# Kernel tuning notes

Hardware: AMD Instinct MI355X
Metric: run time of the kernel (lower is better)

The kernel has to match this reference:

```python
import jax, jax.numpy as jnp
import numpy as np

B, N, M, DIM, H, DH = 2, 2048, 2048, 512, 8, 64
INNER = H * DH  # 512


def setup_inputs() -> dict:
    key = jax.random.key(0)
    ks = jax.random.split(key, 9)
    s = 0.02
    return {
        "x": jax.random.normal(ks[0], (B, N, DIM), jnp.float32),
        "x1": jax.random.normal(ks[1], (B, M, DIM), jnp.float32),
        "attn_mat": jax.random.normal(ks[2], (B, H, N, M), jnp.float32),
        "dots_para": jax.random.uniform(ks[3], (1,), jnp.float32),
        "mat_para": jax.random.uniform(ks[4], (1,), jnp.float32),
        "W_qv": jax.random.normal(ks[5], (DIM, 2 * INNER), jnp.float32) * s,
        "W_k": jax.random.normal(ks[6], (DIM, INNER), jnp.float32) * s,
        "W_out": jax.random.normal(ks[7], (INNER, DIM), jnp.float32) * s,
        "b_out": jax.random.normal(ks[8], (DIM,), jnp.float32) * s,
    }


def _split_heads(t):
    # [b, n, h*d] -> [b, h, n, d]
    b, n, _ = t.shape
    return t.reshape(b, n, H, DH).transpose(0, 2, 1, 3)


def reference(x, x1, attn_mat, dots_para, mat_para, W_qv, W_k, W_out, b_out):
    scale = DH ** -0.5
    qv = x @ W_qv                      # [b, n, 2*inner]
    q, v = jnp.split(qv, 2, axis=-1)
    q = _split_heads(q)                # [b, h, n, d]
    v = _split_heads(v)                # [b, h, n, d]
    k = _split_heads(x1 @ W_k)         # [b, h, m, d]
    dots = jnp.einsum("bhnd,bhmd->bhnm", q, k) * scale
    dots = dots * dots_para + attn_mat * mat_para
    attn = jax.nn.softmax(dots, axis=-1)
    out = jnp.einsum("bhnm,bhmd->bhnd", attn, v)
    out = out.transpose(0, 2, 1, 3).reshape(x.shape[0], x.shape[1], INNER)
    return out @ W_out + b_out
```

## Files before the change

kernel.cpp:

```cpp
#include <hip/hip_runtime.h>
#include <hip/hip_bf16.h>

#define NB 2048
#define MB 2048

typedef __attribute__((ext_vector_type(8))) short short8;
typedef __attribute__((ext_vector_type(4))) float floatx4;

__device__ __forceinline__ unsigned short f2bf(float f) {
    union { float f; unsigned int u; } v; v.f = f;
    unsigned int r = (v.u + 0x7FFFu + ((v.u >> 16) & 1u)) >> 16;
    return (unsigned short)r;
}

__device__ __forceinline__ int swz(int row, int k) {
    return (row << 6) + ((((k >> 3) ^ (row & 7))) << 3) + (k & 7);
}
__device__ __forceinline__ int vswz(int row, int k) {
    return (row << 6) + ((((k >> 3) ^ (row & 7) ^ ((row >> 3) & 7))) << 3) + (k & 7);
}

__launch_bounds__(256)
__global__ void cvt_bf16(const float* __restrict__ in, unsigned short* __restrict__ out, int n4) {
    int idx = blockIdx.x * 256 + threadIdx.x;
    if (idx >= n4) return;
    float4 d = *(const float4*)(in + (size_t)idx * 4);
    uint2 o;
    o.x = (unsigned int)f2bf(d.x) | ((unsigned int)f2bf(d.y) << 16);
    o.y = (unsigned int)f2bf(d.z) | ((unsigned int)f2bf(d.w) << 16);
    *(uint2*)(out + (size_t)idx * 4) = o;
}

__launch_bounds__(256)
__global__ void transpose_cvt(const float* __restrict__ W, unsigned short* __restrict__ Wt,
                              int K, int N) {
    __shared__ float t[64][65];
    const int tid = threadIdx.x;
    const int k0 = blockIdx.x * 64, n0 = blockIdx.y * 64;
#pragma unroll
    for (int p = 0; p < 4; p++) {
        int idx = p * 256 + tid;
        int kr = idx >> 4, c4 = (idx & 15) << 2;
        float4 d = *(const float4*)(W + (size_t)(k0 + kr) * N + n0 + c4);
        t[kr][c4 + 0] = d.x; t[kr][c4 + 1] = d.y; t[kr][c4 + 2] = d.z; t[kr][c4 + 3] = d.w;
    }
    __syncthreads();
#pragma unroll
    for (int p = 0; p < 4; p++) {
        int idx = p * 256 + tid;
        int nr = idx >> 4, k4 = (idx & 15) << 2;
        uint2 o;
        o.x = (unsigned int)f2bf(t[k4 + 0][nr]) | ((unsigned int)f2bf(t[k4 + 1][nr]) << 16);
        o.y = (unsigned int)f2bf(t[k4 + 2][nr]) | ((unsigned int)f2bf(t[k4 + 3][nr]) << 16);
        *(uint2*)(Wt + (size_t)(n0 + nr) * K + k0 + k4) = o;
    }
}

template <int OUT_BF16>
__launch_bounds__(256)
__global__ void gemm_bt(const unsigned short* __restrict__ A, const unsigned short* __restrict__ Bt,
                        const float* __restrict__ bias, void* __restrict__ Cp, int Nc) {
    __shared__ short Al[64 * 64];
    __shared__ short Bl[64 * 64];

    const int tid = threadIdx.x;
    const int w = tid >> 6, lane = tid & 63;
    const int quad = lane >> 4, c16 = lane & 15;
    const int wr = (w >> 1) * 32, wc = (w & 1) * 32;
    const int m0 = blockIdx.x * 64, n0 = blockIdx.y * 64;

    floatx4 acc[2][2];
#pragma unroll
    for (int i = 0; i < 2; i++)
#pragma unroll
        for (int j = 0; j < 2; j++) acc[i][j] = floatx4{0.f, 0.f, 0.f, 0.f};

    for (int kk = 0; kk < 512; kk += 64) {
        __syncthreads();
#pragma unroll
        for (int p = 0; p < 2; p++) {
            int id = p * 256 + tid;
            int row = id >> 3, c8 = (id & 7) << 3;
            *(uint4*)&Al[swz(row, c8)] = *(const uint4*)(A + (size_t)(m0 + row) * 512 + kk + c8);
            *(uint4*)&Bl[swz(row, c8)] = *(const uint4*)(Bt + (size_t)(n0 + row) * 512 + kk + c8);
        }
        __syncthreads();
#pragma unroll
        for (int kc = 0; kc < 2; kc++) {
            short8 af[2], bf[2];
#pragma unroll
            for (int mt = 0; mt < 2; mt++)
                af[mt] = *(const short8*)&Al[swz(wr + mt * 16 + c16, kc * 32 + quad * 8)];
#pragma unroll
            for (int nt = 0; nt < 2; nt++)
                bf[nt] = *(const short8*)&Bl[swz(wc + nt * 16 + c16, kc * 32 + quad * 8)];
#pragma unroll
            for (int mt = 0; mt < 2; mt++)
#pragma unroll
                for (int nt = 0; nt < 2; nt++)
                    acc[mt][nt] = __builtin_amdgcn_mfma_f32_16x16x32_bf16(af[mt], bf[nt], acc[mt][nt], 0, 0, 0);
        }
    }
#pragma unroll
    for (int mt = 0; mt < 2; mt++)
#pragma unroll
        for (int nt = 0; nt < 2; nt++)
#pragma unroll
            for (int r = 0; r < 4; r++) {
                int row = m0 + wr + mt * 16 + quad * 4 + r;
                int col = n0 + wc + nt * 16 + c16;
                float v = acc[mt][nt][r];
                if (OUT_BF16) {
                    ((unsigned short*)Cp)[(size_t)row * Nc + col] = f2bf(v);
                } else {
                    ((float*)Cp)[(size_t)row * Nc + col] = v + bias[col];
                }
            }
}

__launch_bounds__(256)
__global__ void flash_attn(const unsigned short* __restrict__ qv,
                           const unsigned short* __restrict__ kb,
                           const float* __restrict__ attn_mat,
                           const float* __restrict__ dots_para,
                           const float* __restrict__ mat_para,
                           float* __restrict__ Opart,
                           float* __restrict__ lpart) {
    __shared__ short Qs[64 * 64];
    __shared__ short Ks[64 * 64];
    __shared__ short Vs[64 * 64];
    __shared__ short Ps[4][16 * 64];

    const int tid = threadIdx.x, w = tid >> 6, lane = tid & 63;
    const int quad = lane >> 4, c16 = lane & 15;
    const int q0 = blockIdx.x * 64;
    const int bh = blockIdx.y;
    const int sp = blockIdx.z;
    const int b = bh >> 3, h = bh & 7;
    const int ms = sp * (MB / 2);

    const float mp = mat_para[0];
    const float sdp = dots_para[0] * 0.125f;

    for (int id = tid; id < 512; id += 256) {
        int r = id >> 3, c = id & 7;
        *(uint4*)&Qs[swz(r, c * 8)] =
            *(const uint4*)(qv + (size_t)(b * NB + q0 + r) * 1024 + h * 64 + c * 8);
    }
    __syncthreads();
    short8 qf0 = *(const short8*)&Qs[swz(w * 16 + c16, quad * 8)];
    short8 qf1 = *(const short8*)&Qs[swz(w * 16 + c16, 32 + quad * 8)];

    floatx4 O[4];
    float l[4] = {0.f, 0.f, 0.f, 0.f};
#pragma unroll
    for (int dt = 0; dt < 4; dt++) O[dt] = floatx4{0.f, 0.f, 0.f, 0.f};

    const float* am_base = attn_mat + ((size_t)bh * NB + q0 + w * 16 + quad * 4) * MB;

    for (int m0 = ms; m0 < ms + MB / 2; m0 += 64) {
        __syncthreads();
        for (int id = tid; id < 512; id += 256) {
            int r = id >> 3, c = id & 7;
            *(uint4*)&Ks[swz(r, c * 8)] =
                *(const uint4*)(kb + (size_t)(b * MB + m0 + r) * 512 + h * 64 + c * 8);
        }
        for (int id = tid; id < 512; id += 256) {
            int r = id >> 3, c = id & 7;
            uint4 d = *(const uint4*)(qv + (size_t)(b * NB + m0 + r) * 1024 + 512 + h * 64 + c * 8);
            Vs[vswz(c * 8 + 0, r)] = (short)(d.x & 0xffff);
            Vs[vswz(c * 8 + 1, r)] = (short)(d.x >> 16);
            Vs[vswz(c * 8 + 2, r)] = (short)(d.y & 0xffff);
            Vs[vswz(c * 8 + 3, r)] = (short)(d.y >> 16);
            Vs[vswz(c * 8 + 4, r)] = (short)(d.z & 0xffff);
            Vs[vswz(c * 8 + 5, r)] = (short)(d.z >> 16);
            Vs[vswz(c * 8 + 6, r)] = (short)(d.w & 0xffff);
            Vs[vswz(c * 8 + 7, r)] = (short)(d.w >> 16);
        }
        __syncthreads();

        float am[4][4];
#pragma unroll
        for (int t = 0; t < 4; t++)
#pragma unroll
            for (int r = 0; r < 4; r++)
                am[t][r] = am_base[(size_t)r * MB + m0 + t * 16 + c16];

        floatx4 S[4];
#pragma unroll
        for (int t = 0; t < 4; t++) {
            short8 kf0 = *(const short8*)&Ks[swz(t * 16 + c16, quad * 8)];
            short8 kf1 = *(const short8*)&Ks[swz(t * 16 + c16, 32 + quad * 8)];
            floatx4 s = floatx4{0.f, 0.f, 0.f, 0.f};
            s = __builtin_amdgcn_mfma_f32_16x16x32_bf16(qf0, kf0, s, 0, 0, 0);
            s = __builtin_amdgcn_mfma_f32_16x16x32_bf16(qf1, kf1, s, 0, 0, 0);
            S[t] = s;
        }

#pragma unroll
        for (int t = 0; t < 4; t++)
#pragma unroll
            for (int r = 0; r < 4; r++) {
                float p = __expf(fmaf(S[t][r], sdp, am[t][r] * mp));
                l[r] += p;
                Ps[w][swz(quad * 4 + r, t * 16 + c16)] = (short)f2bf(p);
            }
        __threadfence_block();
        short8 pf0 = *(const short8*)&Ps[w][swz(c16, quad * 8)];
        short8 pf1 = *(const short8*)&Ps[w][swz(c16, 32 + quad * 8)];

#pragma unroll
        for (int dt = 0; dt < 4; dt++) {
            short8 vf0 = *(const short8*)&Vs[vswz(dt * 16 + c16, quad * 8)];
            short8 vf1 = *(const short8*)&Vs[vswz(dt * 16 + c16, 32 + quad * 8)];
            O[dt] = __builtin_amdgcn_mfma_f32_16x16x32_bf16(pf0, vf0, O[dt], 0, 0, 0);
            O[dt] = __builtin_amdgcn_mfma_f32_16x16x32_bf16(pf1, vf1, O[dt], 0, 0, 0);
        }
    }

#pragma unroll
    for (int r = 0; r < 4; r++) {
        float s = l[r];
        s += __shfl_xor(s, 1);
        s += __shfl_xor(s, 2);
        s += __shfl_xor(s, 4);
        s += __shfl_xor(s, 8);
        l[r] = s;
    }
    if (c16 == 0) {
#pragma unroll
        for (int r = 0; r < 4; r++)
            lpart[((size_t)(sp * 16 + bh)) * NB + q0 + w * 16 + quad * 4 + r] = l[r];
    }
#pragma unroll
    for (int dt = 0; dt < 4; dt++)
#pragma unroll
        for (int r = 0; r < 4; r++) {
            size_t row = (size_t)sp * 4096 + b * NB + q0 + w * 16 + quad * 4 + r;
            Opart[row * 512 + h * 64 + dt * 16 + c16] = O[dt][r];
        }
}

__launch_bounds__(256)
__global__ void combine_splits(const float* __restrict__ Opart, const float* __restrict__ lpart,
                               unsigned short* __restrict__ ao) {
    int idx = blockIdx.x * 256 + threadIdx.x;
    int row = idx >> 7;
    int col = (idx & 127) << 2;
    int b = row >> 11, n = row & 2047, h = col >> 6;
    float l0 = lpart[(size_t)(b * 8 + h) * NB + n];
    float l1 = lpart[(size_t)(16 + b * 8 + h) * NB + n];
    float rinv = 1.0f / (l0 + l1);
    float4 o0 = *(const float4*)(Opart + (size_t)row * 512 + col);
    float4 o1 = *(const float4*)(Opart + ((size_t)4096 + row) * 512 + col);
    uint2 o;
    o.x = (unsigned int)f2bf((o0.x + o1.x) * rinv) | ((unsigned int)f2bf((o0.y + o1.y) * rinv) << 16);
    o.y = (unsigned int)f2bf((o0.z + o1.z) * rinv) | ((unsigned int)f2bf((o0.w + o1.w) * rinv) << 16);
    *(uint2*)(ao + (size_t)row * 512 + col) = o;
}

extern "C" void kernel_launch(void* const* d_in, const int* in_sizes, int n_in,
                              void* d_out, int out_size, void* d_ws, size_t ws_size,
                              hipStream_t stream) {
    const float* x         = (const float*)d_in[0];
    const float* x1        = (const float*)d_in[1];
    const float* attn_mat  = (const float*)d_in[2];
    const float* dots_para = (const float*)d_in[3];
    const float* mat_para  = (const float*)d_in[4];
    const float* W_qv      = (const float*)d_in[5];
    const float* W_k       = (const float*)d_in[6];
    const float* W_out     = (const float*)d_in[7];
    const float* b_out     = (const float*)d_in[8];
    float* out = (float*)d_out;

    unsigned short* xb    = (unsigned short*)d_ws;
    unsigned short* x1b   = xb    + (size_t)4096 * 512;
    unsigned short* qvbf  = x1b   + (size_t)4096 * 512;
    unsigned short* kbf   = qvbf  + (size_t)4096 * 1024;
    unsigned short* aobf  = kbf   + (size_t)4096 * 512;
    unsigned short* Wqvt  = aobf  + (size_t)4096 * 512;
    unsigned short* Wkt   = Wqvt  + (size_t)1024 * 512;
    unsigned short* Woutt = Wkt   + (size_t)512 * 512;
    float*          Opart = (float*)(Woutt + (size_t)512 * 512);
    float*          lpart = Opart + (size_t)2 * 4096 * 512;

    dim3 blk(256);
    cvt_bf16<<<2048, blk, 0, stream>>>(x, xb, 524288);
    cvt_bf16<<<2048, blk, 0, stream>>>(x1, x1b, 524288);
    transpose_cvt<<<dim3(8, 16), blk, 0, stream>>>(W_qv, Wqvt, 512, 1024);
    transpose_cvt<<<dim3(8, 8), blk, 0, stream>>>(W_k, Wkt, 512, 512);
    transpose_cvt<<<dim3(8, 8), blk, 0, stream>>>(W_out, Woutt, 512, 512);
    gemm_bt<1><<<dim3(64, 16), blk, 0, stream>>>(xb, Wqvt, nullptr, qvbf, 1024);
    gemm_bt<1><<<dim3(64, 8), blk, 0, stream>>>(x1b, Wkt, nullptr, kbf, 512);
    flash_attn<<<dim3(32, 16, 2), blk, 0, stream>>>(qvbf, kbf, attn_mat, dots_para, mat_para, Opart, lpart);
    combine_splits<<<2048, blk, 0, stream>>>(Opart, lpart, aobf);
    gemm_bt<0><<<dim3(64, 8), blk, 0, stream>>>(aobf, Woutt, b_out, out, 512);
}
```

Baseline: 464.6 us.

## Restructure attention with 128-row tiles, double-buffered K/V, 4 splits, fused prep/GEMM launches

Each flash-attention block now covers 128 query rows, two 16-row tiles per wave, so every K/V tile loaded into shared memory is reused twice. K/V and attn_mat loads are register-prefetched and shared memory is double-buffered, so the next tile's global loads overlap the current tile's MFMA work. exp is rewritten as exp2 with log2e folded into the scales. The key dimension is split four ways instead of two. The conversion, transpose and QV/K GEMM launches are merged into fewer kernels to cut launch overhead, at the cost of more partial-output traffic in the combine step and higher register pressure.

```diff
diff --git a/kernel.cpp b/kernel.cpp
--- a/kernel.cpp
+++ b/kernel.cpp
@@ -3,6 +3,8 @@
 
 #define NB 2048
 #define MB 2048
+#define SPLITS 4
+#define MSP (MB / SPLITS)
 
 typedef __attribute__((ext_vector_type(8))) short short8;
 typedef __attribute__((ext_vector_type(4))) float floatx4;
@@ -21,22 +23,34 @@
 }
 
 __launch_bounds__(256)
-__global__ void cvt_bf16(const float* __restrict__ in, unsigned short* __restrict__ out, int n4) {
-    int idx = blockIdx.x * 256 + threadIdx.x;
-    if (idx >= n4) return;
-    float4 d = *(const float4*)(in + (size_t)idx * 4);
-    uint2 o;
-    o.x = (unsigned int)f2bf(d.x) | ((unsigned int)f2bf(d.y) << 16);
-    o.y = (unsigned int)f2bf(d.z) | ((unsigned int)f2bf(d.w) << 16);
-    *(uint2*)(out + (size_t)idx * 4) = o;
-}
-
-__launch_bounds__(256)
-__global__ void transpose_cvt(const float* __restrict__ W, unsigned short* __restrict__ Wt,
-                              int K, int N) {
+__global__ void prep(const float* __restrict__ x, const float* __restrict__ x1,
+                     const float* __restrict__ Wqv, const float* __restrict__ Wk,
+                     const float* __restrict__ Wout,
+                     unsigned short* __restrict__ xb, unsigned short* __restrict__ x1b,
+                     unsigned short* __restrict__ Wqvt, unsigned short* __restrict__ Wkt,
+                     unsigned short* __restrict__ Woutt) {
     __shared__ float t[64][65];
-    const int tid = threadIdx.x;
-    const int k0 = blockIdx.x * 64, n0 = blockIdx.y * 64;
+    const int bid = blockIdx.x, tid = threadIdx.x;
+    if (bid < 2048) {
+        const float* in = bid < 1024 ? x : x1;
+        unsigned short* out = bid < 1024 ? xb : x1b;
+        size_t off = ((size_t)(bid & 1023) * 256 + tid) * 8;
+        float4 d0 = *(const float4*)(in + off);
+        float4 d1 = *(const float4*)(in + off + 4);
+        uint4 o;
+        o.x = (unsigned int)f2bf(d0.x) | ((unsigned int)f2bf(d0.y) << 16);
+        o.y = (unsigned int)f2bf(d0.z) | ((unsigned int)f2bf(d0.w) << 16);
+        o.z = (unsigned int)f2bf(d1.x) | ((unsigned int)f2bf(d1.y) << 16);
+        o.w = (unsigned int)f2bf(d1.z) | ((unsigned int)f2bf(d1.w) << 16);
+        *(uint4*)(out + off) = o;
+        return;
+    }
+    int tb = bid - 2048;
+    const float* W; unsigned short* Wt; int N;
+    if (tb < 128)      { W = Wqv;  Wt = Wqvt;  N = 1024; }
+    else if (tb < 192) { tb -= 128; W = Wk;   Wt = Wkt;   N = 512; }
+    else               { tb -= 192; W = Wout; Wt = Woutt; N = 512; }
+    const int k0 = (tb & 7) * 64, n0 = (tb >> 3) * 64;
 #pragma unroll
     for (int p = 0; p < 4; p++) {
         int idx = p * 256 + tid;
@@ -52,22 +66,20 @@
         uint2 o;
         o.x = (unsigned int)f2bf(t[k4 + 0][nr]) | ((unsigned int)f2bf(t[k4 + 1][nr]) << 16);
         o.y = (unsigned int)f2bf(t[k4 + 2][nr]) | ((unsigned int)f2bf(t[k4 + 3][nr]) << 16);
-        *(uint2*)(Wt + (size_t)(n0 + nr) * K + k0 + k4) = o;
+        *(uint2*)(Wt + (size_t)(n0 + nr) * 512 + k0 + k4) = o;
     }
 }
 
 template <int OUT_BF16>
-__launch_bounds__(256)
-__global__ void gemm_bt(const unsigned short* __restrict__ A, const unsigned short* __restrict__ Bt,
-                        const float* __restrict__ bias, void* __restrict__ Cp, int Nc) {
-    __shared__ short Al[64 * 64];
-    __shared__ short Bl[64 * 64];
-
+__device__ __forceinline__ void gemm64_body(const unsigned short* __restrict__ A,
+                                            const unsigned short* __restrict__ Bt,
+                                            const float* __restrict__ bias,
+                                            void* __restrict__ Cp, int Nc, int m0, int n0,
+                                            short* Al, short* Bl) {
     const int tid = threadIdx.x;
     const int w = tid >> 6, lane = tid & 63;
     const int quad = lane >> 4, c16 = lane & 15;
     const int wr = (w >> 1) * 32, wc = (w & 1) * 32;
-    const int m0 = blockIdx.x * 64, n0 = blockIdx.y * 64;
 
     floatx4 acc[2][2];
 #pragma unroll
@@ -119,6 +131,29 @@
 }
 
 __launch_bounds__(256)
+__global__ void gemm_qvk(const unsigned short* __restrict__ xb, const unsigned short* __restrict__ x1b,
+                         const unsigned short* __restrict__ Wqvt, const unsigned short* __restrict__ Wkt,
+                         unsigned short* __restrict__ qvbf, unsigned short* __restrict__ kbf) {
+    __shared__ short Al[64 * 64];
+    __shared__ short Bl[64 * 64];
+    int bid = blockIdx.x;
+    if (bid < 1024) {
+        gemm64_body<1>(xb, Wqvt, nullptr, qvbf, 1024, (bid & 63) * 64, (bid >> 6) * 64, Al, Bl);
+    } else {
+        bid -= 1024;
+        gemm64_body<1>(x1b, Wkt, nullptr, kbf, 512, (bid & 63) * 64, (bid >> 6) * 64, Al, Bl);
+    }
+}
+
+__launch_bounds__(256)
+__global__ void gemm_out(const unsigned short* __restrict__ A, const unsigned short* __restrict__ Bt,
+                         const float* __restrict__ bias, float* __restrict__ C) {
+    __shared__ short Al[64 * 64];
+    __shared__ short Bl[64 * 64];
+    gemm64_body<0>(A, Bt, bias, C, 512, blockIdx.x * 64, blockIdx.y * 64, Al, Bl);
+}
+
+__launch_bounds__(256)
 __global__ void flash_attn(const unsigned short* __restrict__ qv,
                            const unsigned short* __restrict__ kb,
                            const float* __restrict__ attn_mat,
@@ -126,119 +161,167 @@
                            const float* __restrict__ mat_para,
                            float* __restrict__ Opart,
                            float* __restrict__ lpart) {
-    __shared__ short Qs[64 * 64];
-    __shared__ short Ks[64 * 64];
-    __shared__ short Vs[64 * 64];
-    __shared__ short Ps[4][16 * 64];
+    __shared__ short QP[4][32 * 64];
+    __shared__ short Ks[2][64 * 64];
+    __shared__ short Vs[2][64 * 64];
 
     const int tid = threadIdx.x, w = tid >> 6, lane = tid & 63;
     const int quad = lane >> 4, c16 = lane & 15;
-    const int q0 = blockIdx.x * 64;
+    const int q0 = blockIdx.x * 128;
     const int bh = blockIdx.y;
     const int sp = blockIdx.z;
     const int b = bh >> 3, h = bh & 7;
-    const int ms = sp * (MB / 2);
-
-    const float mp = mat_para[0];
-    const float sdp = dots_para[0] * 0.125f;
-
-    for (int id = tid; id < 512; id += 256) {
+    const int ms = sp * MSP;
+
+    const float log2e = 1.4426950408889634f;
+    const float mp = mat_para[0] * log2e;
+    const float sdp = dots_para[0] * 0.125f * log2e;
+
+    short* QPf = (short*)QP;
+#pragma unroll
+    for (int p = 0; p < 4; p++) {
+        int id = p * 256 + tid;
         int r = id >> 3, c = id & 7;
-        *(uint4*)&Qs[swz(r, c * 8)] =
+        *(uint4*)&QPf[swz(r, c * 8)] =
             *(const uint4*)(qv + (size_t)(b * NB + q0 + r) * 1024 + h * 64 + c * 8);
     }
     __syncthreads();
-    short8 qf0 = *(const short8*)&Qs[swz(w * 16 + c16, quad * 8)];
-    short8 qf1 = *(const short8*)&Qs[swz(w * 16 + c16, 32 + quad * 8)];
-
-    floatx4 O[4];
-    float l[4] = {0.f, 0.f, 0.f, 0.f};
-#pragma unroll
-    for (int dt = 0; dt < 4; dt++) O[dt] = floatx4{0.f, 0.f, 0.f, 0.f};
-
-    const float* am_base = attn_mat + ((size_t)bh * NB + q0 + w * 16 + quad * 4) * MB;
-
-    for (int m0 = ms; m0 < ms + MB / 2; m0 += 64) {
+    short8 qf[2][2];
+#pragma unroll
+    for (int at = 0; at < 2; at++)
+#pragma unroll
+        for (int kc = 0; kc < 2; kc++)
+            qf[at][kc] = *(const short8*)&QPf[swz(w * 32 + at * 16 + c16, kc * 32 + quad * 8)];
+    short* Pw = &QPf[w * 2048];
+
+    const int sr = tid >> 3, sc = tid & 7;
+    uint4 kreg[2], vreg[2];
+    auto loadKV = [&](int m) {
+#pragma unroll
+        for (int p = 0; p < 2; p++) {
+            int r = p * 32 + sr;
+            kreg[p] = *(const uint4*)(kb + (size_t)(b * MB + m + r) * 512 + h * 64 + sc * 8);
+            vreg[p] = *(const uint4*)(qv + (size_t)(b * NB + m + r) * 1024 + 512 + h * 64 + sc * 8);
+        }
+    };
+    auto storeKV = [&](int bufi) {
+#pragma unroll
+        for (int p = 0; p < 2; p++) {
+            int r = p * 32 + sr;
+            *(uint4*)&Ks[bufi][swz(r, sc * 8)] = kreg[p];
+            uint4 d = vreg[p];
+            Vs[bufi][vswz(sc * 8 + 0, r)] = (short)(d.x & 0xffff);
+            Vs[bufi][vswz(sc * 8 + 1, r)] = (short)(d.x >> 16);
+            Vs[bufi][vswz(sc * 8 + 2, r)] = (short)(d.y & 0xffff);
+            Vs[bufi][vswz(sc * 8 + 3, r)] = (short)(d.y >> 16);
+            Vs[bufi][vswz(sc * 8 + 4, r)] = (short)(d.z & 0xffff);
+            Vs[bufi][vswz(sc * 8 + 5, r)] = (short)(d.z >> 16);
+            Vs[bufi][vswz(sc * 8 + 6, r)] = (short)(d.w & 0xffff);
+            Vs[bufi][vswz(sc * 8 + 7, r)] = (short)(d.w >> 16);
+        }
+    };
+    const float* amp = attn_mat + ((size_t)bh * NB + q0 + w * 32 + quad * 4) * MB + c16;
+    float amr[2][4][4];
+    auto loadAM = [&](int m0_) {
+#pragma unroll
+        for (int at = 0; at < 2; at++)
+#pragma unroll
+            for (int r = 0; r < 4; r++)
+#pragma unroll
+                for (int t = 0; t < 4; t++)
+                    amr[at][t][r] = amp[(size_t)(at * 16 + r) * MB + m0_ + t * 16];
+    };
+
+    loadKV(ms);
+    storeKV(0);
+    loadKV(ms + 64 < ms + MSP ? ms + 64 : ms);
+    loadAM(ms);
+
+    floatx4 O[2][4];
+    float l[2][4];
+#pragma unroll
+    for (int at = 0; at < 2; at++)
+#pragma unroll
+        for (int i = 0; i < 4; i++) { O[at][i] = floatx4{0.f, 0.f, 0.f, 0.f}; l[at][i] = 0.f; }
+
+    for (int it = 0; it < MSP / 64; it++) {
+        const int m0 = ms + it * 64;
+        const int buf = it & 1, nbuf = buf ^ 1;
         __syncthreads();
-        for (int id = tid; id < 512; id += 256) {
-            int r = id >> 3, c = id & 7;
-            *(uint4*)&Ks[swz(r, c * 8)] =
-                *(const uint4*)(kb + (size_t)(b * MB + m0 + r) * 512 + h * 64 + c * 8);
-        }
-        for (int id = tid; id < 512; id += 256) {
-            int r = id >> 3, c = id & 7;
-            uint4 d = *(const uint4*)(qv + (size_t)(b * NB + m0 + r) * 1024 + 512 + h * 64 + c * 8);
-            Vs[vswz(c * 8 + 0, r)] = (short)(d.x & 0xffff);
-            Vs[vswz(c * 8 + 1, r)] = (short)(d.x >> 16);
-            Vs[vswz(c * 8 + 2, r)] = (short)(d.y & 0xffff);
-            Vs[vswz(c * 8 + 3, r)] = (short)(d.y >> 16);
-            Vs[vswz(c * 8 + 4, r)] = (short)(d.z & 0xffff);
-            Vs[vswz(c * 8 + 5, r)] = (short)(d.z >> 16);
-            Vs[vswz(c * 8 + 6, r)] = (short)(d.w & 0xffff);
-            Vs[vswz(c * 8 + 7, r)] = (short)(d.w >> 16);
-        }
-        __syncthreads();
-
-        float am[4][4];
-#pragma unroll
-        for (int t = 0; t < 4; t++)
+        storeKV(nbuf);
+        int mnn = m0 + 128; if (mnn >= ms + MSP) mnn = ms;
+        loadKV(mnn);
+
+        floatx4 S[2][4];
+#pragma unroll
+        for (int t = 0; t < 4; t++) {
+            short8 kf0 = *(const short8*)&Ks[buf][swz(t * 16 + c16, quad * 8)];
+            short8 kf1 = *(const short8*)&Ks[buf][swz(t * 16 + c16, 32 + quad * 8)];
+#pragma unroll
+            for (int at = 0; at < 2; at++) {
+                floatx4 s = floatx4{0.f, 0.f, 0.f, 0.f};
+                s = __builtin_amdgcn_mfma_f32_16x16x32_bf16(qf[at][0], kf0, s, 0, 0, 0);
+                s = __builtin_amdgcn_mfma_f32_16x16x32_bf16(qf[at][1], kf1, s, 0, 0, 0);
+                S[at][t] = s;
+            }
+        }
+
+#pragma unroll
+        for (int at = 0; at < 2; at++)
+#pragma unroll
+            for (int t = 0; t < 4; t++)
+#pragma unroll
+                for (int r = 0; r < 4; r++) {
+                    float p = exp2f(fmaf(S[at][t][r], sdp, amr[at][t][r] * mp));
+                    l[at][r] += p;
+                    Pw[swz(at * 16 + quad * 4 + r, t * 16 + c16)] = (short)f2bf(p);
+                }
+        int mnx = m0 + 64; if (mnx >= ms + MSP) mnx = ms;
+        loadAM(mnx);
+        __threadfence_block();
+
+        short8 pf[2][2];
+#pragma unroll
+        for (int at = 0; at < 2; at++)
+#pragma unroll
+            for (int kc = 0; kc < 2; kc++)
+                pf[at][kc] = *(const short8*)&Pw[swz(at * 16 + c16, kc * 32 + quad * 8)];
+#pragma unroll
+        for (int dt = 0; dt < 4; dt++) {
+            short8 vf0 = *(const short8*)&Vs[buf][vswz(dt * 16 + c16, quad * 8)];
+            short8 vf1 = *(const short8*)&Vs[buf][vswz(dt * 16 + c16, 32 + quad * 8)];
+#pragma unroll
+            for (int at = 0; at < 2; at++) {
+                O[at][dt] = __builtin_amdgcn_mfma_f32_16x16x32_bf16(pf[at][0], vf0, O[at][dt], 0, 0, 0);
+                O[at][dt] = __builtin_amdgcn_mfma_f32_16x16x32_bf16(pf[at][1], vf1, O[at][dt], 0, 0, 0);
+            }
+        }
+    }
+
+#pragma unroll
+    for (int at = 0; at < 2; at++) {
+#pragma unroll
+        for (int r = 0; r < 4; r++) {
+            float s = l[at][r];
+            s += __shfl_xor(s, 1);
+            s += __shfl_xor(s, 2);
+            s += __shfl_xor(s, 4);
+            s += __shfl_xor(s, 8);
+            l[at][r] = s;
+        }
+        if (c16 == 0) {
 #pragma unroll
             for (int r = 0; r < 4; r++)
-                am[t][r] = am_base[(size_t)r * MB + m0 + t * 16 + c16];
-
-        floatx4 S[4];
-#pragma unroll
-        for (int t = 0; t < 4; t++) {
-            short8 kf0 = *(const short8*)&Ks[swz(t * 16 + c16, quad * 8)];
-            short8 kf1 = *(const short8*)&Ks[swz(t * 16 + c16, 32 + quad * 8)];
-            floatx4 s = floatx4{0.f, 0.f, 0.f, 0.f};
-            s = __builtin_amdgcn_mfma_f32_16x16x32_bf16(qf0, kf0, s, 0, 0, 0);
-            s = __builtin_amdgcn_mfma_f32_16x16x32_bf16(qf1, kf1, s, 0, 0, 0);
-            S[t] = s;
-        }
-
-#pragma unroll
-        for (int t = 0; t < 4; t++)
+                lpart[(size_t)(sp * 16 + bh) * NB + q0 + w * 32 + at * 16 + quad * 4 + r] = l[at][r];
+        }
+#pragma unroll
+        for (int dt = 0; dt < 4; dt++)
 #pragma unroll
             for (int r = 0; r < 4; r++) {
-                float p = __expf(fmaf(S[t][r], sdp, am[t][r] * mp));
-                l[r] += p;
-                Ps[w][swz(quad * 4 + r, t * 16 + c16)] = (short)f2bf(p);
+                size_t row = (size_t)sp * 4096 + b * NB + q0 + w * 32 + at * 16 + quad * 4 + r;
+                Opart[row * 512 + h * 64 + dt * 16 + c16] = O[at][dt][r];
             }
-        __threadfence_block();
-        short8 pf0 = *(const short8*)&Ps[w][swz(c16, quad * 8)];
-        short8 pf1 = *(const short8*)&Ps[w][swz(c16, 32 + quad * 8)];
-
-#pragma unroll
-        for (int dt = 0; dt < 4; dt++) {
-            short8 vf0 = *(const short8*)&Vs[vswz(dt * 16 + c16, quad * 8)];
-            short8 vf1 = *(const short8*)&Vs[vswz(dt * 16 + c16, 32 + quad * 8)];
-            O[dt] = __builtin_amdgcn_mfma_f32_16x16x32_bf16(pf0, vf0, O[dt], 0, 0, 0);
-            O[dt] = __builtin_amdgcn_mfma_f32_16x16x32_bf16(pf1, vf1, O[dt], 0, 0, 0);
-        }
-    }
-
-#pragma unroll
-    for (int r = 0; r < 4; r++) {
-        float s = l[r];
-        s += __shfl_xor(s, 1);
-        s += __shfl_xor(s, 2);
-        s += __shfl_xor(s, 4);
-        s += __shfl_xor(s, 8);
-        l[r] = s;
-    }
-    if (c16 == 0) {
-#pragma unroll
-        for (int r = 0; r < 4; r++)
-            lpart[((size_t)(sp * 16 + bh)) * NB + q0 + w * 16 + quad * 4 + r] = l[r];
-    }
-#pragma unroll
-    for (int dt = 0; dt < 4; dt++)
-#pragma unroll
-        for (int r = 0; r < 4; r++) {
-            size_t row = (size_t)sp * 4096 + b * NB + q0 + w * 16 + quad * 4 + r;
-            Opart[row * 512 + h * 64 + dt * 16 + c16] = O[dt][r];
-        }
+    }
 }
 
 __launch_bounds__(256)
@@ -248,15 +331,19 @@
     int row = idx >> 7;
     int col = (idx & 127) << 2;
     int b = row >> 11, n = row & 2047, h = col >> 6;
-    float l0 = lpart[(size_t)(b * 8 + h) * NB + n];
-    float l1 = lpart[(size_t)(16 + b * 8 + h) * NB + n];
-    float rinv = 1.0f / (l0 + l1);
-    float4 o0 = *(const float4*)(Opart + (size_t)row * 512 + col);
-    float4 o1 = *(const float4*)(Opart + ((size_t)4096 + row) * 512 + col);
-    uint2 o;
-    o.x = (unsigned int)f2bf((o0.x + o1.x) * rinv) | ((unsigned int)f2bf((o0.y + o1.y) * rinv) << 16);
-    o.y = (unsigned int)f2bf((o0.z + o1.z) * rinv) | ((unsigned int)f2bf((o0.w + o1.w) * rinv) << 16);
-    *(uint2*)(ao + (size_t)row * 512 + col) = o;
+    float ls = 0.f;
+    float4 o = {0.f, 0.f, 0.f, 0.f};
+#pragma unroll
+    for (int sp = 0; sp < SPLITS; sp++) {
+        ls += lpart[(size_t)(sp * 16 + b * 8 + h) * NB + n];
+        float4 os = *(const float4*)(Opart + ((size_t)sp * 4096 + row) * 512 + col);
+        o.x += os.x; o.y += os.y; o.z += os.z; o.w += os.w;
+    }
+    float rinv = 1.0f / ls;
+    uint2 pk;
+    pk.x = (unsigned int)f2bf(o.x * rinv) | ((unsigned int)f2bf(o.y * rinv) << 16);
+    pk.y = (unsigned int)f2bf(o.z * rinv) | ((unsigned int)f2bf(o.w * rinv) << 16);
+    *(uint2*)(ao + (size_t)row * 512 + col) = pk;
 }
 
 extern "C" void kernel_launch(void* const* d_in, const int* in_sizes, int n_in,
@@ -282,17 +369,12 @@
     unsigned short* Wkt   = Wqvt  + (size_t)1024 * 512;
     unsigned short* Woutt = Wkt   + (size_t)512 * 512;
     float*          Opart = (float*)(Woutt + (size_t)512 * 512);
-    float*          lpart = Opart + (size_t)2 * 4096 * 512;
+    float*          lpart = Opart + (size_t)SPLITS * 4096 * 512;
 
     dim3 blk(256);
-    cvt_bf16<<<2048, blk, 0, stream>>>(x, xb, 524288);
-    cvt_bf16<<<2048, blk, 0, stream>>>(x1, x1b, 524288);
-    transpose_cvt<<<dim3(8, 16), blk, 0, stream>>>(W_qv, Wqvt, 512, 1024);
-    transpose_cvt<<<dim3(8, 8), blk, 0, stream>>>(W_k, Wkt, 512, 512);
-    transpose_cvt<<<dim3(8, 8), blk, 0, stream>>>(W_out, Woutt, 512, 512);
-    gemm_bt<1><<<dim3(64, 16), blk, 0, stream>>>(xb, Wqvt, nullptr, qvbf, 1024);
-    gemm_bt<1><<<dim3(64, 8), blk, 0, stream>>>(x1b, Wkt, nullptr, kbf, 512);
-    flash_attn<<<dim3(32, 16, 2), blk, 0, stream>>>(qvbf, kbf, attn_mat, dots_para, mat_para, Opart, lpart);
+    prep<<<2304, blk, 0, stream>>>(x, x1, W_qv, W_k, W_out, xb, x1b, Wqvt, Wkt, Woutt);
+    gemm_qvk<<<1536, blk, 0, stream>>>(xb, x1b, Wqvt, Wkt, qvbf, kbf);
+    flash_attn<<<dim3(16, 16, SPLITS), blk, 0, stream>>>(qvbf, kbf, attn_mat, dots_para, mat_para, Opart, lpart);
     combine_splits<<<2048, blk, 0, stream>>>(Opart, lpart, aobf);
-    gemm_bt<0><<<dim3(64, 8), blk, 0, stream>>>(aobf, Woutt, b_out, out, 512);
-}
+    gemm_out<<<dim3(64, 8), blk, 0, stream>>>(aobf, Woutt, b_out, out);
+}
```

After: 449.8 us. 1.03x faster.
